# Optimization experiments

Measured on AMD Instinct MI355X. Metric: run time of the kernel, lower is better.

## Reference

```python
import jax, jax.numpy as jnp
import numpy as np

L, D, F, H, K, V, E = 15, 512, 2048, 64, 128, 30, 1024
DH = D // H  # 8
B, N = 8, 128


def _ln(x, s, b, eps=1e-5):
    m = x.mean(-1, keepdims=True)
    v = ((x - m) ** 2).mean(-1, keepdims=True)
    return (x - m) * jax.lax.rsqrt(v + eps) * s + b


def _gauss(x, mean, std):
    # matches torch.jit gaussian(): pi = 3.14159
    a = (2.0 * 3.14159) ** 0.5
    return jnp.exp(-0.5 * ((x - mean) / std) ** 2) / (a * std)


def setup_inputs() -> dict:
    key = jax.random.key(0)
    ks = iter(jax.random.split(key, 48))
    nrm = lambda shape, sc=0.02: jax.random.normal(next(ks), shape, jnp.float32) * sc
    zeros = lambda shape: jnp.zeros(shape, jnp.float32)
    ones = lambda shape: jnp.ones(shape, jnp.float32)
    return dict(
        src_tokens=jax.random.randint(next(ks), (B, N), 0, V),
        src_distance=jax.random.uniform(next(ks), (B, N, N), jnp.float32) * 3.0,
        src_edge_type=jax.random.randint(next(ks), (B, N, N), 0, E),
        token_embed=nrm((V, D)),
        gbf_means=jax.random.uniform(next(ks), (K,), jnp.float32, 0.0, 3.0),
        gbf_stds=jax.random.uniform(next(ks), (K,), jnp.float32, 0.0, 3.0),
        gbf_mul=ones((E, 1)),
        gbf_bias=zeros((E, 1)),
        proj_w1=nrm((K, K)), proj_b1=zeros((K,)),
        proj_w2=nrm((K, H)), proj_b2=zeros((H,)),
        emb_ln_s=ones((D,)), emb_ln_b=zeros((D,)),
        Wq=nrm((L, D, D)), bq=zeros((L, D)),
        Wk=nrm((L, D, D)), bk=zeros((L, D)),
        Wv=nrm((L, D, D)), bv=zeros((L, D)),
        Wo=nrm((L, D, D)), bo=zeros((L, D)),
        ln1_s=ones((L, D)), ln1_b=zeros((L, D)),
        ln2_s=ones((L, D)), ln2_b=zeros((L, D)),
        Wf1=nrm((L, D, F)), bf1=zeros((L, F)),
        Wf2=nrm((L, F, D)), bf2=zeros((L, D)),
        fin_ln_s=ones((D,)), fin_ln_b=zeros((D,)),
    )


def reference(src_tokens, src_distance, src_edge_type, token_embed,
              gbf_means, gbf_stds, gbf_mul, gbf_bias,
              proj_w1, proj_b1, proj_w2, proj_b2,
              emb_ln_s, emb_ln_b,
              Wq, bq, Wk, bk, Wv, bv, Wo, bo,
              ln1_s, ln1_b, ln2_s, ln2_b,
              Wf1, bf1, Wf2, bf2, fin_ln_s, fin_ln_b):
    # --- GaussianLayer: per-pair edge-type affine + K-kernel RBF -> [B,N,N,K]
    mul = gbf_mul[src_edge_type]          # [B,N,N,1]
    add = gbf_bias[src_edge_type]         # [B,N,N,1]
    g = mul * src_distance[..., None] + add
    std = jnp.abs(gbf_stds) + 1e-5
    g = _gauss(g, gbf_means, std)         # broadcast [B,N,N,1] vs [K] -> [B,N,N,K]
    # --- gbf_proj (NonLinearHead K->K->H) -> attention bias [B,H,N,N]
    hproj = jax.nn.gelu(g @ proj_w1 + proj_b1, approximate=False)
    bias0 = jnp.transpose(hproj @ proj_w2 + proj_b2, (0, 3, 1, 2))

    x = _ln(token_embed[src_tokens], emb_ln_s, emb_ln_b)  # [B,N,D]
    scale = DH ** -0.5

    def layer(carry, p):
        x, bias = carry
        wq, bq_, wk, bk_, wv, bv_, wo, bo_, s1, b1, s2, b2, wf1, bf1_, wf2, bf2_ = p
        # pre-LN self-attention with additive pair bias
        r = x
        y = _ln(x, s1, b1)
        q = (y @ wq + bq_).reshape(B, N, H, DH) * scale
        k = (y @ wk + bk_).reshape(B, N, H, DH)
        v = (y @ wv + bv_).reshape(B, N, H, DH)
        scores = jnp.einsum('bihd,bjhd->bhij', q, k) + bias  # [B,H,N,N]
        probs = jax.nn.softmax(scores, axis=-1)
        o = jnp.einsum('bhij,bjhd->bihd', probs, v).reshape(B, N, D)
        x = r + (o @ wo + bo_)
        # pre-LN FFN
        r = x
        y = _ln(x, s2, b2)
        y = jax.nn.gelu(y @ wf1 + bf1_, approximate=False) @ wf2 + bf2_
        # UniMol: pre-softmax scores feed the next layer as its pair bias
        return (r + y, scores), None

    (x, _), _ = jax.lax.scan(
        layer, (x, bias0),
        (Wq, bq, Wk, bk, Wv, bv, Wo, bo, ln1_s, ln1_b, ln2_s, ln2_b, Wf1, bf1, Wf2, bf2))
    return _ln(x, fin_ln_s, fin_ln_b)  # [B,N,D]
```

## Files before the change

### kernel.cpp

```cpp
#include <hip/hip_runtime.h>
#include <hip/hip_bf16.h>

#define Bv 8
#define Nv 128
#define Dv 512
#define Hv 64
#define DHv 8
#define Fv 2048
#define Lv 15
#define Kv 128

typedef unsigned short u16;
typedef __attribute__((ext_vector_type(8))) short s16x8;
typedef __attribute__((ext_vector_type(4))) float f32x4;

__device__ __forceinline__ float b2f(u16 u) {
    union { unsigned int i; float f; } w;
    w.i = ((unsigned int)u) << 16;
    return w.f;
}

__device__ __forceinline__ u16 f2b(float f) {
    __hip_bfloat16 h = __float2bfloat16(f);
    u16 u;
    __builtin_memcpy(&u, &h, 2);
    return u;
}

__device__ __forceinline__ bool probe_bf16(const void* p) {
    return ((const u16*)p)[0] == 0x3F80u;
}

__device__ __forceinline__ float ldv(const u16* p, size_t i)   { return b2f(p[i]); }
__device__ __forceinline__ float ldv(const float* p, size_t i) { return p[i]; }

__device__ __forceinline__ u16 ld16(const u16* p, size_t i)   { return p[i]; }
__device__ __forceinline__ u16 ld16(const float* p, size_t i) { return f2b(p[i]); }

__device__ __forceinline__ float erf_fast(float x) {
    float ax = fabsf(x);
    float tt = 1.0f / fmaf(0.3275911f, ax, 1.0f);
    float y = tt * fmaf(tt, fmaf(tt, fmaf(tt, fmaf(tt, 1.061405429f, -1.453152027f),
                                          1.421413741f), -0.284496736f), 0.254829592f);
    float r = 1.0f - y * __expf(-ax * ax);
    return copysignf(r, x);
}

__device__ __forceinline__ float geluf(float v) {
    return 0.5f * v * (1.0f + erf_fast(v * 0.70710678118654752f));
}

template<typename T>
__device__ __forceinline__ void gbf2_body(
    const T* dist, const int* etype, const T* means, const T* stds,
    const T* mulW, const T* addW, const T* w1, const T* b1w,
    const T* w2, const T* b2w, float* biasOut,
    float* xs, float* smean, float* sinv, u16* GA, u16* Bst)
{
    const int t = threadIdx.x;
    const int iq = blockIdx.x;
    const int j0 = blockIdx.y << 6;
    const int b = blockIdx.z;

    if (t < 64) {
        size_t pidx = ((size_t)(b * Nv + iq)) * Nv + j0 + t;
        int e = etype[pidx];
        xs[t] = ldv(dist, pidx) * ldv(mulW, e) + ldv(addW, e);
    } else if (t >= 128) {
        int k = t - 128;
        float sv = fabsf(ldv(stds, k)) + 1e-5f;
        smean[k] = ldv(means, k);
        sinv[k] = 1.0f / sv;
    }
    __syncthreads();

    const int w = t >> 6, l = t & 63;
    const int lg = l >> 4, lr = l & 15;
    const int wm = (w >> 1) << 5;
    const int wn1 = (w & 1) << 6;
    const int mt0 = wm >> 4;

    const int b1col = t & 127, b1lg0 = (t >> 7) << 1;

    s16x8 rb0, rb1;
    {
        union { s16x8 v; u16 u[8]; } p0, p1;
        #pragma unroll
        for (int j = 0; j < 8; j++) {
            p0.u[j] = ld16(w1, (size_t)((b1lg0 + 0) * 8 + j) * Kv + b1col);
            p1.u[j] = ld16(w1, (size_t)((b1lg0 + 1) * 8 + j) * Kv + b1col);
        }
        rb0 = p0.v; rb1 = p1.v;
    }

    {
        const int row = t & 63;
        const int kc = t >> 6;
        const float x = xs[row];
        const int mt = row >> 4, r = row & 15;
        #pragma unroll
        for (int lg2 = 0; lg2 < 4; lg2++) {
            union { s16x8 v; u16 u[8]; } pk;
            #pragma unroll
            for (int j = 0; j < 8; j++) {
                int k = kc * 32 + lg2 * 8 + j;
                float z = (x - smean[k]) * sinv[k];
                pk.u[j] = f2b(__expf(-0.5f * z * z) * (0.39894261f * sinv[k]));
            }
            *reinterpret_cast<s16x8*>(&GA[(((mt * 4 + kc) * 4 + lg2) * 16 + r) << 3]) = pk.v;
        }
    }
    __syncthreads();

    f32x4 acc1[2][4];
    #pragma unroll
    for (int mi = 0; mi < 2; mi++)
        #pragma unroll
        for (int ni = 0; ni < 4; ni++) acc1[mi][ni] = (f32x4){0.f, 0.f, 0.f, 0.f};

    for (int kc = 0; kc < 4; kc++) {
        *reinterpret_cast<s16x8*>(
            &Bst[((((b1col >> 4) * 4 + b1lg0 + 0) * 16 + (b1col & 15)) << 3)]) = rb0;
        *reinterpret_cast<s16x8*>(
            &Bst[((((b1col >> 4) * 4 + b1lg0 + 1) * 16 + (b1col & 15)) << 3)]) = rb1;
        __syncthreads();

        if (kc < 3) {
            union { s16x8 v; u16 u[8]; } p0, p1;
            #pragma unroll
            for (int j = 0; j < 8; j++) {
                p0.u[j] = ld16(w1, (size_t)((kc + 1) * 32 + (b1lg0 + 0) * 8 + j) * Kv + b1col);
                p1.u[j] = ld16(w1, (size_t)((kc + 1) * 32 + (b1lg0 + 1) * 8 + j) * Kv + b1col);
            }
            rb0 = p0.v; rb1 = p1.v;
        }

        s16x8 a0 = *reinterpret_cast<const s16x8*>(&GA[((((mt0 + 0) * 4 + kc) * 4 + lg) * 16 + lr) << 3]);
        s16x8 a1 = *reinterpret_cast<const s16x8*>(&GA[((((mt0 + 1) * 4 + kc) * 4 + lg) * 16 + lr) << 3]);
        #pragma unroll
        for (int ni = 0; ni < 4; ni++) {
            int nt = (wn1 >> 4) + ni;
            s16x8 bf = *reinterpret_cast<const s16x8*>(&Bst[((nt * 4 + lg) * 16 + lr) << 3]);
            acc1[0][ni] = __builtin_amdgcn_mfma_f32_16x16x32_bf16(a0, bf, acc1[0][ni], 0, 0, 0);
            acc1[1][ni] = __builtin_amdgcn_mfma_f32_16x16x32_bf16(a1, bf, acc1[1][ni], 0, 0, 0);
        }
        __syncthreads();
    }

    const int b2col = t & 63, b2lg = t >> 6;
    s16x8 rc;
    {
        union { s16x8 v; u16 u[8]; } pb;
        #pragma unroll
        for (int j = 0; j < 8; j++)
            pb.u[j] = ld16(w2, (size_t)(b2lg * 8 + j) * Hv + b2col);
        rc = pb.v;
    }

    #pragma unroll
    for (int mi = 0; mi < 2; mi++) {
        #pragma unroll
        for (int ni = 0; ni < 4; ni++) {
            int col = wn1 + ni * 16 + lr;
            float bb = ldv(b1w, col);
            #pragma unroll
            for (int i = 0; i < 4; i++) {
                int row = wm + mi * 16 + lg * 4 + i;
                float v = geluf(acc1[mi][ni][i] + bb);
                GA[((((row >> 4) * 4 + (col >> 5)) * 4 + ((col >> 3) & 3)) * 16 + (row & 15)) * 8 + (col & 7)] = f2b(v);
            }
        }
    }
    __syncthreads();

    const int wn2 = (w & 1) << 5;

    f32x4 acc2[2][2];
    #pragma unroll
    for (int mi = 0; mi < 2; mi++)
        #pragma unroll
        for (int ni = 0; ni < 2; ni++) acc2[mi][ni] = (f32x4){0.f, 0.f, 0.f, 0.f};

    for (int kc = 0; kc < 4; kc++) {
        *reinterpret_cast<s16x8*>(
            &Bst[((((b2col >> 4) * 4 + b2lg) * 16 + (b2col & 15)) << 3)]) = rc;
        __syncthreads();

        if (kc < 3) {
            union { s16x8 v; u16 u[8]; } pb;
            #pragma unroll
            for (int j = 0; j < 8; j++)
                pb.u[j] = ld16(w2, (size_t)((kc + 1) * 32 + b2lg * 8 + j) * Hv + b2col);
            rc = pb.v;
        }

        s16x8 a0 = *reinterpret_cast<const s16x8*>(&GA[((((mt0 + 0) * 4 + kc) * 4 + lg) * 16 + lr) << 3]);
        s16x8 a1 = *reinterpret_cast<const s16x8*>(&GA[((((mt0 + 1) * 4 + kc) * 4 + lg) * 16 + lr) << 3]);
        #pragma unroll
        for (int ni = 0; ni < 2; ni++) {
            int nt = (wn2 >> 4) + ni;
            s16x8 bf = *reinterpret_cast<const s16x8*>(&Bst[((nt * 4 + lg) * 16 + lr) << 3]);
            acc2[0][ni] = __builtin_amdgcn_mfma_f32_16x16x32_bf16(a0, bf, acc2[0][ni], 0, 0, 0);
            acc2[1][ni] = __builtin_amdgcn_mfma_f32_16x16x32_bf16(a1, bf, acc2[1][ni], 0, 0, 0);
        }
        __syncthreads();
    }

    #pragma unroll
    for (int mi = 0; mi < 2; mi++) {
        #pragma unroll
        for (int ni = 0; ni < 2; ni++) {
            int h = wn2 + ni * 16 + lr;
            int jb = wm + mi * 16 + lg * 4;
            float badd = ldv(b2w, h);
            size_t oidx = (((size_t)(b * Hv + h)) * Nv + iq) * Nv + j0 + jb;
            *reinterpret_cast<float4*>(&biasOut[oidx]) =
                make_float4(acc2[mi][ni][0] + badd, acc2[mi][ni][1] + badd,
                            acc2[mi][ni][2] + badd, acc2[mi][ni][3] + badd);
        }
    }
}

__global__ __launch_bounds__(256) void gbf2_k(
    const void* dist, const int* etype, const void* means, const void* stds,
    const void* mulW, const void* addW, const void* w1, const void* b1,
    const void* w2, const void* b2, float* biasOut, const void* probe)
{
    __shared__ float xs[64];
    __shared__ float smean[Kv];
    __shared__ float sinv[Kv];
    __shared__ __align__(16) u16 GA[8192];
    __shared__ __align__(16) u16 Bst[4096];
    if (probe_bf16(probe))
        gbf2_body<u16>((const u16*)dist, etype, (const u16*)means, (const u16*)stds,
                       (const u16*)mulW, (const u16*)addW, (const u16*)w1, (const u16*)b1,
                       (const u16*)w2, (const u16*)b2, biasOut, xs, smean, sinv, GA, Bst);
    else
        gbf2_body<float>((const float*)dist, etype, (const float*)means, (const float*)stds,
                         (const float*)mulW, (const float*)addW, (const float*)w1, (const float*)b1,
                         (const float*)w2, (const float*)b2, biasOut, xs, smean, sinv, GA, Bst);
}

__device__ __forceinline__ void block_stats_512(float x0, float x1, float& mean, float& rstd)
{
    float sum = x0 + x1, sq = x0 * x0 + x1 * x1;
    #pragma unroll
    for (int off = 32; off; off >>= 1) {
        sum += __shfl_xor(sum, off);
        sq  += __shfl_xor(sq, off);
    }
    __shared__ float ssum[4], ssq[4];
    int t = threadIdx.x;
    if ((t & 63) == 0) { ssum[t >> 6] = sum; ssq[t >> 6] = sq; }
    __syncthreads();
    sum = ssum[0] + ssum[1] + ssum[2] + ssum[3];
    sq  = ssq[0] + ssq[1] + ssq[2] + ssq[3];
    mean = sum * (1.0f / 512.0f);
    float var = sq * (1.0f / 512.0f) - mean * mean;
    rstd = rsqrtf(var + 1e-5f);
}

template<typename T>
__device__ __forceinline__ void embed_body(
    const int* toks, const T* emb, const T* sc, const T* bi, float* xout)
{
    int row = blockIdx.x, t = threadIdx.x;
    int tok = toks[row];
    float x0 = ldv(emb, (size_t)tok * Dv + t);
    float x1 = ldv(emb, (size_t)tok * Dv + t + 256);
    float mean, rstd;
    block_stats_512(x0, x1, mean, rstd);
    xout[(size_t)row * Dv + t]       = (x0 - mean) * rstd * ldv(sc, t) + ldv(bi, t);
    xout[(size_t)row * Dv + t + 256] = (x1 - mean) * rstd * ldv(sc, t + 256) + ldv(bi, t + 256);
}

__global__ __launch_bounds__(256) void embed_ln_k(
    const int* toks, const void* emb, const void* sc, const void* bi,
    float* xout, const void* probe)
{
    if (probe_bf16(probe))
        embed_body<u16>(toks, (const u16*)emb, (const u16*)sc, (const u16*)bi, xout);
    else
        embed_body<float>(toks, (const float*)emb, (const float*)sc, (const float*)bi, xout);
}

template<typename T>
__device__ __forceinline__ void ln_body(
    const float* xin, const T* sc, const T* bi, size_t pofs, u16* yout)
{
    int row = blockIdx.x, t = threadIdx.x;
    const float* xp = xin + (size_t)row * Dv;
    float x0 = xp[t], x1 = xp[t + 256];
    float mean, rstd;
    block_stats_512(x0, x1, mean, rstd);
    yout[(size_t)row * Dv + t]       = f2b((x0 - mean) * rstd * ldv(sc, pofs + t) + ldv(bi, pofs + t));
    yout[(size_t)row * Dv + t + 256] = f2b((x1 - mean) * rstd * ldv(sc, pofs + t + 256) + ldv(bi, pofs + t + 256));
}

__global__ __launch_bounds__(256) void ln_k(
    const float* xin, const void* sc, const void* bi, unsigned long long pofs,
    u16* yout, const void* probe)
{
    if (probe_bf16(probe))
        ln_body<u16>(xin, (const u16*)sc, (const u16*)bi, (size_t)pofs, yout);
    else
        ln_body<float>(xin, (const float*)sc, (const float*)bi, (size_t)pofs, yout);
}

template<typename T, bool OUT_BF>
__device__ __forceinline__ void final_ln_body(
    const float* xin, const T* sc, const T* bi, void* yout)
{
    int row = blockIdx.x, t = threadIdx.x;
    const float* xp = xin + (size_t)row * Dv;
    float x0 = xp[t], x1 = xp[t + 256];
    float mean, rstd;
    block_stats_512(x0, x1, mean, rstd);
    float o0 = (x0 - mean) * rstd * ldv(sc, t) + ldv(bi, t);
    float o1 = (x1 - mean) * rstd * ldv(sc, t + 256) + ldv(bi, t + 256);
    if (OUT_BF) {
        __hip_bfloat16* yp = (__hip_bfloat16*)yout;
        yp[(size_t)row * Dv + t]       = __float2bfloat16(o0);
        yp[(size_t)row * Dv + t + 256] = __float2bfloat16(o1);
    } else {
        float* yp = (float*)yout;
        yp[(size_t)row * Dv + t]       = o0;
        yp[(size_t)row * Dv + t + 256] = o1;
    }
}

__global__ __launch_bounds__(256) void final_ln_k(
    const float* xin, const void* sc, const void* bi, void* yout, const void* probe)
{
    if (probe_bf16(probe))
        final_ln_body<u16, true>(xin, (const u16*)sc, (const u16*)bi, yout);
    else
        final_ln_body<float, false>(xin, (const float*)sc, (const float*)bi, yout);
}

template<typename T>
__device__ __forceinline__ void gemm_mfma_body(
    const u16* A, const T* W, const T* bias, const float* R,
    void* C, int Nc, int Kc, int act, int res, int kbegin, int kend,
    int raw, int cbf, u16* Al, u16* Bl)
{
    const int tid = threadIdx.x;
    const int l = tid & 63, w = tid >> 6;
    const int wm = (w >> 1) << 5, wn = (w & 1) << 5;
    const int bm = blockIdx.y * 64, bn = blockIdx.x * 64;
    const int lg = l >> 4, lr = l & 15;
    const int mt0 = wm >> 4, nt0 = wn >> 4;

    f32x4 acc00 = {}, acc01 = {}, acc10 = {}, acc11 = {};

    const int arow = tid >> 2, akq = tid & 3;
    const u16* aGp = A + (size_t)(bm + arow) * Kc + (akq << 3);
    const int aL0 = ((((arow >> 4) * 2 + 0) * 4 + akq) * 16 + (arow & 15)) << 3;
    const int aL1 = ((((arow >> 4) * 2 + 1) * 4 + akq) * 16 + (arow & 15)) << 3;

    const int bcol = tid & 63;
    const int be = tid >> 6;
    const int bc = be >> 1, blg0 = (be & 1) << 1;
    const int bnt = bcol >> 4, bcl = bcol & 15;
    const int bL0 = (((bnt * 2 + bc) * 4 + blg0) * 16 + bcl) << 3;
    const int bL1 = (((bnt * 2 + bc) * 4 + blg0 + 1) * 16 + bcl) << 3;

    s16x8 ra0, ra1, rb0, rb1;
    ra0 = *reinterpret_cast<const s16x8*>(aGp + kbegin);
    ra1 = *reinterpret_cast<const s16x8*>(aGp + kbegin + 32);
    {
        union { s16x8 v; u16 u[8]; } p0, p1;
        #pragma unroll
        for (int j = 0; j < 8; j++) {
            p0.u[j] = ld16(W, (size_t)(kbegin + bc * 32 + blg0 * 8 + j) * Nc + bn + bcol);
            p1.u[j] = ld16(W, (size_t)(kbegin + bc * 32 + blg0 * 8 + 8 + j) * Nc + bn + bcol);
        }
        rb0 = p0.v; rb1 = p1.v;
    }

    for (int kt = kbegin; kt < kend; kt += 64) {
        *reinterpret_cast<s16x8*>(&Al[aL0]) = ra0;
        *reinterpret_cast<s16x8*>(&Al[aL1]) = ra1;
        *reinterpret_cast<s16x8*>(&Bl[bL0]) = rb0;
        *reinterpret_cast<s16x8*>(&Bl[bL1]) = rb1;
        __syncthreads();

        const int kn = kt + 64;
        if (kn < kend) {
            ra0 = *reinterpret_cast<const s16x8*>(aGp + kn);
            ra1 = *reinterpret_cast<const s16x8*>(aGp + kn + 32);
            union { s16x8 v; u16 u[8]; } p0, p1;
            #pragma unroll
            for (int j = 0; j < 8; j++) {
                p0.u[j] = ld16(W, (size_t)(kn + bc * 32 + blg0 * 8 + j) * Nc + bn + bcol);
                p1.u[j] = ld16(W, (size_t)(kn + bc * 32 + blg0 * 8 + 8 + j) * Nc + bn + bcol);
            }
            rb0 = p0.v; rb1 = p1.v;
        }

        #pragma unroll
        for (int c = 0; c < 2; c++) {
            s16x8 af0 = *reinterpret_cast<const s16x8*>(&Al[((((mt0 + 0) * 2 + c) * 4 + lg) * 16 + lr) << 3]);
            s16x8 af1 = *reinterpret_cast<const s16x8*>(&Al[((((mt0 + 1) * 2 + c) * 4 + lg) * 16 + lr) << 3]);
            s16x8 bf0 = *reinterpret_cast<const s16x8*>(&Bl[((((nt0 + 0) * 2 + c) * 4 + lg) * 16 + lr) << 3]);
            s16x8 bf1 = *reinterpret_cast<const s16x8*>(&Bl[((((nt0 + 1) * 2 + c) * 4 + lg) * 16 + lr) << 3]);
            acc00 = __builtin_amdgcn_mfma_f32_16x16x32_bf16(af0, bf0, acc00, 0, 0, 0);
            acc01 = __builtin_amdgcn_mfma_f32_16x16x32_bf16(af0, bf1, acc01, 0, 0, 0);
            acc10 = __builtin_amdgcn_mfma_f32_16x16x32_bf16(af1, bf0, acc10, 0, 0, 0);
            acc11 = __builtin_amdgcn_mfma_f32_16x16x32_bf16(af1, bf1, acc11, 0, 0, 0);
        }
        __syncthreads();
    }

    #pragma unroll
    for (int mi = 0; mi < 2; mi++) {
        #pragma unroll
        for (int i = 0; i < 4; i++) {
            const int row = bm + wm + mi * 16 + lg * 4 + i;
            const float* Rrow = res ? (R + (size_t)row * Nc) : nullptr;
            #pragma unroll
            for (int ni = 0; ni < 2; ni++) {
                const int col = bn + wn + ni * 16 + lr;
                float cv = (ni == 0) ? (mi == 0 ? acc00[i] : acc10[i])
                                     : (mi == 0 ? acc01[i] : acc11[i]);
                if (raw) {
                    ((float*)C)[(size_t)row * Nc + col] = cv;
                } else {
                    cv += ldv(bias, col);
                    if (act) cv = geluf(cv);
                    if (res) cv += Rrow[col];
                    if (cbf) ((u16*)C)[(size_t)row * Nc + col] = f2b(cv);
                    else     ((float*)C)[(size_t)row * Nc + col] = cv;
                }
            }
        }
    }
}

__global__ __launch_bounds__(256) void gemm_k(
    const u16* A, const void* W, unsigned long long wofs,
    const void* bias, unsigned long long bofs, const float* R,
    void* C, int Nc, int Kc, int act, int res, int cbf, const void* probe)
{
    __shared__ __align__(16) u16 Al[4096];
    __shared__ __align__(16) u16 Bl[4096];
    const int nz = gridDim.z, z = blockIdx.z;
    const int kchunk = Kc / nz;
    const int kbegin = z * kchunk, kend = kbegin + kchunk;
    const int raw = (nz > 1) ? 1 : 0;
    void* Cz = (char*)C + (size_t)z * ((size_t)gridDim.y * 64) * Nc * sizeof(float);
    if (probe_bf16(probe))
        gemm_mfma_body<u16>(A, (const u16*)W + wofs, (const u16*)bias + bofs, R, Cz,
                            Nc, Kc, act, res, kbegin, kend, raw, cbf, Al, Bl);
    else
        gemm_mfma_body<float>(A, (const float*)W + wofs, (const float*)bias + bofs, R, Cz,
                              Nc, Kc, act, res, kbegin, kend, raw, cbf, Al, Bl);
}

__global__ __launch_bounds__(256) void qkv_k(
    const u16* A,
    const void* W0, const void* W1p, const void* W2p, unsigned long long wofs,
    const void* b0, const void* b1p, const void* b2p, unsigned long long bofs,
    float* C0, float* C1, float* C2, const void* probe)
{
    __shared__ __align__(16) u16 Al[4096];
    __shared__ __align__(16) u16 Bl[4096];
    const int z = blockIdx.z;
    const void* W  = (z == 0) ? W0 : (z == 1) ? W1p : W2p;
    const void* bb = (z == 0) ? b0 : (z == 1) ? b1p : b2p;
    float* C       = (z == 0) ? C0 : (z == 1) ? C1 : C2;
    if (probe_bf16(probe))
        gemm_mfma_body<u16>(A, (const u16*)W + wofs, (const u16*)bb + bofs, nullptr, C,
                            Dv, Dv, 0, 0, 0, Dv, 0, 0, Al, Bl);
    else
        gemm_mfma_body<float>(A, (const float*)W + wofs, (const float*)bb + bofs, nullptr, C,
                              Dv, Dv, 0, 0, 0, Dv, 0, 0, Al, Bl);
}

template<typename T>
__device__ __forceinline__ void combln_body(
    const float* parts, const T* pbias, float* X,
    const T* lnS, const T* lnB, size_t pofs, u16* Y)
{
    const int t = threadIdx.x;
    const int rowb = t >> 7;
    const int col = (t & 127) << 2;
    const int row = (blockIdx.x << 1) + rowb;
    const size_t idx = (size_t)row * Dv + col;

    float4 sv = *reinterpret_cast<const float4*>(&parts[idx]);
    #pragma unroll
    for (int p = 1; p < 4; p++) {
        const float4 q2 = *reinterpret_cast<const float4*>(&parts[(size_t)p * 524288 + idx]);
        sv.x += q2.x; sv.y += q2.y; sv.z += q2.z; sv.w += q2.w;
    }
    sv.x += ldv(pbias, col);     sv.y += ldv(pbias, col + 1);
    sv.z += ldv(pbias, col + 2); sv.w += ldv(pbias, col + 3);
    const float4 r = *reinterpret_cast<const float4*>(&X[idx]);
    sv.x += r.x; sv.y += r.y; sv.z += r.z; sv.w += r.w;
    *reinterpret_cast<float4*>(&X[idx]) = sv;

    float sum = sv.x + sv.y + sv.z + sv.w;
    float sq  = sv.x * sv.x + sv.y * sv.y + sv.z * sv.z + sv.w * sv.w;
    #pragma unroll
    for (int off = 32; off; off >>= 1) {
        sum += __shfl_xor(sum, off);
        sq  += __shfl_xor(sq, off);
    }
    __shared__ float ssum[4], ssq[4];
    const int wv = t >> 6;
    if ((t & 63) == 0) { ssum[wv] = sum; ssq[wv] = sq; }
    __syncthreads();
    sum = ssum[rowb * 2] + ssum[rowb * 2 + 1];
    sq  = ssq[rowb * 2] + ssq[rowb * 2 + 1];
    const float mean = sum * (1.0f / 512.0f);
    const float var = sq * (1.0f / 512.0f) - mean * mean;
    const float rstd = rsqrtf(var + 1e-5f);

    ushort4 yv;
    yv.x = f2b((sv.x - mean) * rstd * ldv(lnS, pofs + col)     + ldv(lnB, pofs + col));
    yv.y = f2b((sv.y - mean) * rstd * ldv(lnS, pofs + col + 1) + ldv(lnB, pofs + col + 1));
    yv.z = f2b((sv.z - mean) * rstd * ldv(lnS, pofs + col + 2) + ldv(lnB, pofs + col + 2));
    yv.w = f2b((sv.w - mean) * rstd * ldv(lnS, pofs + col + 3) + ldv(lnB, pofs + col + 3));
    *reinterpret_cast<ushort4*>(&Y[idx]) = yv;
}

__global__ __launch_bounds__(256) void combln_k(
    const float* parts, const void* pbias, unsigned long long bofs, float* X,
    const void* lnS, const void* lnB, unsigned long long pofs, u16* Y,
    const void* probe)
{
    if (probe_bf16(probe))
        combln_body<u16>(parts, (const u16*)pbias + bofs, X,
                         (const u16*)lnS, (const u16*)lnB, (size_t)pofs, Y);
    else
        combln_body<float>(parts, (const float*)pbias + bofs, X,
                           (const float*)lnS, (const float*)lnB, (size_t)pofs, Y);
}

__global__ __launch_bounds__(512) void attn_k(
    const float* __restrict__ q, const float* __restrict__ k, const float* __restrict__ v,
    float* bias, u16* __restrict__ o)
{
    __shared__ __align__(16) float ks[Nv][DHv];
    __shared__ __align__(16) float vs[Nv][DHv];

    const int t = threadIdx.x;
    const int h = blockIdx.x;
    const int b = blockIdx.y;
    const int i = (blockIdx.z << 6) + (t >> 3);
    const int e = t & 7;
    const float scale = 0.35355339059327373f;

    const float* kh = k + (size_t)(b * Nv) * Dv + h * DHv;
    const float* vh = v + (size_t)(b * Nv) * Dv + h * DHv;

    {
        const int j = t >> 2, c = (t & 3) << 1;
        const float2 k2 = *reinterpret_cast<const float2*>(kh + (size_t)j * Dv + c);
        const float2 v2 = *reinterpret_cast<const float2*>(vh + (size_t)j * Dv + c);
        *reinterpret_cast<float2*>(&ks[j][c]) = k2;
        *reinterpret_cast<float2*>(&vs[j][c]) = v2;
    }

    const float* qp = q + (size_t)(b * Nv + i) * Dv + h * DHv;
    const float4 q0 = *reinterpret_cast<const float4*>(qp);
    const float4 q1 = *reinterpret_cast<const float4*>(qp + 4);

    float* bp = bias + (((size_t)(b * Hv + h)) * Nv + i) * Nv;

    float s[16];
    #pragma unroll
    for (int w = 0; w < 16; w++) s[w] = bp[(w << 3) + e];

    __syncthreads();

    float mx = -1e30f;
    #pragma unroll
    for (int w = 0; w < 16; w++) {
        const int j = (w << 3) + e;
        const float4 k0 = *reinterpret_cast<const float4*>(&ks[j][0]);
        const float4 k1 = *reinterpret_cast<const float4*>(&ks[j][4]);
        float d = q0.x * k0.x + q0.y * k0.y + q0.z * k0.z + q0.w * k0.w +
                  q1.x * k1.x + q1.y * k1.y + q1.z * k1.z + q1.w * k1.w;
        float val = s[w] + scale * d;
        s[w] = val;
        bp[j] = val;
        mx = fmaxf(mx, val);
    }

    mx = fmaxf(mx, __shfl_xor(mx, 1));
    mx = fmaxf(mx, __shfl_xor(mx, 2));
    mx = fmaxf(mx, __shfl_xor(mx, 4));

    float sum = 0.0f;
    #pragma unroll
    for (int w = 0; w < 16; w++) {
        s[w] = __expf(s[w] - mx);
        sum += s[w];
    }
    sum += __shfl_xor(sum, 1);
    sum += __shfl_xor(sum, 2);
    sum += __shfl_xor(sum, 4);
    const float inv = 1.0f / sum;

    float a0 = 0, a1 = 0, a2 = 0, a3 = 0, a4 = 0, a5 = 0, a6 = 0, a7 = 0;
    #pragma unroll
    for (int w = 0; w < 16; w++) {
        const int j = (w << 3) + e;
        const float4 v0 = *reinterpret_cast<const float4*>(&vs[j][0]);
        const float4 v1 = *reinterpret_cast<const float4*>(&vs[j][4]);
        const float p = s[w];
        a0 += p * v0.x; a1 += p * v0.y; a2 += p * v0.z; a3 += p * v0.w;
        a4 += p * v1.x; a5 += p * v1.y; a6 += p * v1.z; a7 += p * v1.w;
    }
    a0 += __shfl_xor(a0, 1); a0 += __shfl_xor(a0, 2); a0 += __shfl_xor(a0, 4);
    a1 += __shfl_xor(a1, 1); a1 += __shfl_xor(a1, 2); a1 += __shfl_xor(a1, 4);
    a2 += __shfl_xor(a2, 1); a2 += __shfl_xor(a2, 2); a2 += __shfl_xor(a2, 4);
    a3 += __shfl_xor(a3, 1); a3 += __shfl_xor(a3, 2); a3 += __shfl_xor(a3, 4);
    a4 += __shfl_xor(a4, 1); a4 += __shfl_xor(a4, 2); a4 += __shfl_xor(a4, 4);
    a5 += __shfl_xor(a5, 1); a5 += __shfl_xor(a5, 2); a5 += __shfl_xor(a5, 4);
    a6 += __shfl_xor(a6, 1); a6 += __shfl_xor(a6, 2); a6 += __shfl_xor(a6, 4);
    a7 += __shfl_xor(a7, 1); a7 += __shfl_xor(a7, 2); a7 += __shfl_xor(a7, 4);

    if (e == 0) {
        u16* op = o + (size_t)(b * Nv + i) * Dv + h * DHv;
        ushort4 o0 = { f2b(a0 * inv), f2b(a1 * inv), f2b(a2 * inv), f2b(a3 * inv) };
        ushort4 o1 = { f2b(a4 * inv), f2b(a5 * inv), f2b(a6 * inv), f2b(a7 * inv) };
        *reinterpret_cast<ushort4*>(op)     = o0;
        *reinterpret_cast<ushort4*>(op + 4) = o1;
    }
}

extern "C" void kernel_launch(void* const* d_in, const int* in_sizes, int n_in,
                              void* d_out, int out_size, void* d_ws, size_t ws_size,
                              hipStream_t stream)
{
    const int*  src_tokens = (const int*)d_in[0];
    const void* src_dist   = d_in[1];
    const int*  src_edge   = (const int*)d_in[2];
    const void* token_emb  = d_in[3];
    const void* gbf_means  = d_in[4];
    const void* gbf_stds   = d_in[5];
    const void* gbf_mul    = d_in[6];
    const void* gbf_bias   = d_in[7];
    const void* pw1        = d_in[8];
    const void* pb1        = d_in[9];
    const void* pw2        = d_in[10];
    const void* pb2        = d_in[11];
    const void* embs       = d_in[12];
    const void* embb       = d_in[13];
    const void* Wq         = d_in[14];
    const void* bq         = d_in[15];
    const void* Wk         = d_in[16];
    const void* bk         = d_in[17];
    const void* Wv         = d_in[18];
    const void* bvp        = d_in[19];
    const void* Wo         = d_in[20];
    const void* bo         = d_in[21];
    const void* ln1s       = d_in[22];
    const void* ln1b       = d_in[23];
    const void* ln2s       = d_in[24];
    const void* ln2b       = d_in[25];
    const void* Wf1        = d_in[26];
    const void* bf1        = d_in[27];
    const void* Wf2        = d_in[28];
    const void* bf2        = d_in[29];
    const void* fins       = d_in[30];
    const void* finb       = d_in[31];
    const void* probe      = embs;

    float* ws   = (float*)d_ws;
    float* x    = ws;
    float* y    = x  + 524288;
    float* qb   = y  + 524288;
    float* kb   = qb + 524288;
    float* vb   = kb + 524288;
    float* ob   = vb + 524288;
    float* hb   = ob + 524288;
    u16*   hbf  = (u16*)hb;
    u16*   ybf  = (u16*)(hb + 1048576);
    u16*   obf  = (u16*)(hb + 1310720);
    float* bias = hb + 2097152;

    gbf2_k<<<dim3(Nv, 2, Bv), 256, 0, stream>>>(
        src_dist, src_edge, gbf_means, gbf_stds, gbf_mul, gbf_bias,
        pw1, pb1, pw2, pb2, bias, probe);
    embed_ln_k<<<Bv * Nv, 256, 0, stream>>>(src_tokens, token_emb, embs, embb, x, probe);
    ln_k<<<Bv * Nv, 256, 0, stream>>>(x, ln1s, ln1b, 0ull, ybf, probe);

    dim3 gQKV(512 / 64, 1024 / 64, 3);
    dim3 gS4(512 / 64, 1024 / 64, 4);
    dim3 gF1(2048 / 64, 1024 / 64);
    for (int l = 0; l < Lv; l++) {
        unsigned long long wofs  = (unsigned long long)l * Dv * Dv;
        unsigned long long wofsF = (unsigned long long)l * Dv * Fv;
        unsigned long long dof   = (unsigned long long)l * Dv;
        unsigned long long fof   = (unsigned long long)l * Fv;
        unsigned long long nofs  = (l + 1 < Lv) ? (unsigned long long)(l + 1) * Dv : 0ull;

        qkv_k<<<gQKV, 256, 0, stream>>>(ybf, Wq, Wk, Wv, wofs, bq, bk, bvp, dof,
                                        qb, kb, vb, probe);
        attn_k<<<dim3(Hv, Bv, 2), 512, 0, stream>>>(qb, kb, vb, bias, obf);
        gemm_k<<<gS4, 256, 0, stream>>>(obf, Wo, wofs, bo, dof, nullptr, y, 512, 512, 0, 0, 0, probe);
        combln_k<<<512, 256, 0, stream>>>(y, bo, dof, x, ln2s, ln2b, dof, ybf, probe);
        gemm_k<<<gF1, 256, 0, stream>>>(ybf, Wf1, wofsF, bf1, fof, nullptr, hbf, 2048, 512, 1, 0, 1, probe);
        gemm_k<<<gS4, 256, 0, stream>>>(hbf, Wf2, wofsF, bf2, fof, nullptr, y, 512, 2048, 0, 0, 0, probe);
        combln_k<<<512, 256, 0, stream>>>(y, bf2, dof, x, ln1s, ln1b, nofs, ybf, probe);
    }
    final_ln_k<<<Bv * Nv, 256, 0, stream>>>(x, fins, finb, d_out, probe);
}
```

Baseline: 1.460 ms.

## Double-buffer GEMM LDS tiles and split-K the QKV projection into attention

The shared GEMM body now ping-pongs between two LDS buffers, so the next K-tile is written to the alternate buffer after the MFMAs and only one barrier is needed per iteration. The QKV kernel is split along K into two halves (six z-slices instead of three), which doubles the number of blocks. It writes raw partial sums into spare workspace buffers. The attention kernel then adds the two partials and the q/k/v biases when it loads them. This trades extra LDS per block (lower occupancy) and extra partial-sum traffic for more parallelism and less barrier stalling.

```diff
diff --git a/kernel.cpp b/kernel.cpp
--- a/kernel.cpp
+++ b/kernel.cpp
@@ -377,16 +377,17 @@
         }
         rb0 = p0.v; rb1 = p1.v;
     }
-
+    *reinterpret_cast<s16x8*>(&Al[aL0]) = ra0;
+    *reinterpret_cast<s16x8*>(&Al[aL1]) = ra1;
+    *reinterpret_cast<s16x8*>(&Bl[bL0]) = rb0;
+    *reinterpret_cast<s16x8*>(&Bl[bL1]) = rb1;
+    __syncthreads();
+
+    int cur = 0;
     for (int kt = kbegin; kt < kend; kt += 64) {
-        *reinterpret_cast<s16x8*>(&Al[aL0]) = ra0;
-        *reinterpret_cast<s16x8*>(&Al[aL1]) = ra1;
-        *reinterpret_cast<s16x8*>(&Bl[bL0]) = rb0;
-        *reinterpret_cast<s16x8*>(&Bl[bL1]) = rb1;
-        __syncthreads();
-
         const int kn = kt + 64;
-        if (kn < kend) {
+        const bool more = kn < kend;
+        if (more) {
             ra0 = *reinterpret_cast<const s16x8*>(aGp + kn);
             ra1 = *reinterpret_cast<const s16x8*>(aGp + kn + 32);
             union { s16x8 v; u16 u[8]; } p0, p1;
@@ -398,18 +399,28 @@
             rb0 = p0.v; rb1 = p1.v;
         }
 
+        const int co = cur << 12;
         #pragma unroll
         for (int c = 0; c < 2; c++) {
-            s16x8 af0 = *reinterpret_cast<const s16x8*>(&Al[((((mt0 + 0) * 2 + c) * 4 + lg) * 16 + lr) << 3]);
-            s16x8 af1 = *reinterpret_cast<const s16x8*>(&Al[((((mt0 + 1) * 2 + c) * 4 + lg) * 16 + lr) << 3]);
-            s16x8 bf0 = *reinterpret_cast<const s16x8*>(&Bl[((((nt0 + 0) * 2 + c) * 4 + lg) * 16 + lr) << 3]);
-            s16x8 bf1 = *reinterpret_cast<const s16x8*>(&Bl[((((nt0 + 1) * 2 + c) * 4 + lg) * 16 + lr) << 3]);
+            s16x8 af0 = *reinterpret_cast<const s16x8*>(&Al[co + (((((mt0 + 0) * 2 + c) * 4 + lg) * 16 + lr) << 3)]);
+            s16x8 af1 = *reinterpret_cast<const s16x8*>(&Al[co + (((((mt0 + 1) * 2 + c) * 4 + lg) * 16 + lr) << 3)]);
+            s16x8 bf0 = *reinterpret_cast<const s16x8*>(&Bl[co + (((((nt0 + 0) * 2 + c) * 4 + lg) * 16 + lr) << 3)]);
+            s16x8 bf1 = *reinterpret_cast<const s16x8*>(&Bl[co + (((((nt0 + 1) * 2 + c) * 4 + lg) * 16 + lr) << 3)]);
             acc00 = __builtin_amdgcn_mfma_f32_16x16x32_bf16(af0, bf0, acc00, 0, 0, 0);
             acc01 = __builtin_amdgcn_mfma_f32_16x16x32_bf16(af0, bf1, acc01, 0, 0, 0);
             acc10 = __builtin_amdgcn_mfma_f32_16x16x32_bf16(af1, bf0, acc10, 0, 0, 0);
             acc11 = __builtin_amdgcn_mfma_f32_16x16x32_bf16(af1, bf1, acc11, 0, 0, 0);
         }
-        __syncthreads();
+
+        if (more) {
+            const int no = (cur ^ 1) << 12;
+            *reinterpret_cast<s16x8*>(&Al[no + aL0]) = ra0;
+            *reinterpret_cast<s16x8*>(&Al[no + aL1]) = ra1;
+            *reinterpret_cast<s16x8*>(&Bl[no + bL0]) = rb0;
+            *reinterpret_cast<s16x8*>(&Bl[no + bL1]) = rb1;
+            __syncthreads();
+            cur ^= 1;
+        }
     }
 
     #pragma unroll
@@ -442,8 +453,8 @@
     const void* bias, unsigned long long bofs, const float* R,
     void* C, int Nc, int Kc, int act, int res, int cbf, const void* probe)
 {
-    __shared__ __align__(16) u16 Al[4096];
-    __shared__ __align__(16) u16 Bl[4096];
+    __shared__ __align__(16) u16 Al[8192];
+    __shared__ __align__(16) u16 Bl[8192];
     const int nz = gridDim.z, z = blockIdx.z;
     const int kchunk = Kc / nz;
     const int kbegin = z * kchunk, kend = kbegin + kchunk;
@@ -460,21 +471,24 @@
 __global__ __launch_bounds__(256) void qkv_k(
     const u16* A,
     const void* W0, const void* W1p, const void* W2p, unsigned long long wofs,
-    const void* b0, const void* b1p, const void* b2p, unsigned long long bofs,
-    float* C0, float* C1, float* C2, const void* probe)
-{
-    __shared__ __align__(16) u16 Al[4096];
-    __shared__ __align__(16) u16 Bl[4096];
+    float* q0, float* q1, float* k0, float* k1, float* v0, float* v1,
+    const void* probe)
+{
+    __shared__ __align__(16) u16 Al[8192];
+    __shared__ __align__(16) u16 Bl[8192];
     const int z = blockIdx.z;
-    const void* W  = (z == 0) ? W0 : (z == 1) ? W1p : W2p;
-    const void* bb = (z == 0) ? b0 : (z == 1) ? b1p : b2p;
-    float* C       = (z == 0) ? C0 : (z == 1) ? C1 : C2;
+    const int g = z >> 1, half = z & 1;
+    const void* W  = (g == 0) ? W0 : (g == 1) ? W1p : W2p;
+    float* C       = (g == 0) ? (half ? q1 : q0)
+                   : (g == 1) ? (half ? k1 : k0)
+                              : (half ? v1 : v0);
+    const int kbegin = half * 256, kend = kbegin + 256;
     if (probe_bf16(probe))
-        gemm_mfma_body<u16>(A, (const u16*)W + wofs, (const u16*)bb + bofs, nullptr, C,
-                            Dv, Dv, 0, 0, 0, Dv, 0, 0, Al, Bl);
+        gemm_mfma_body<u16>(A, (const u16*)W + wofs, (const u16*)nullptr, nullptr, C,
+                            Dv, Dv, 0, 0, kbegin, kend, 1, 0, Al, Bl);
     else
-        gemm_mfma_body<float>(A, (const float*)W + wofs, (const float*)bb + bofs, nullptr, C,
-                              Dv, Dv, 0, 0, 0, Dv, 0, 0, Al, Bl);
+        gemm_mfma_body<float>(A, (const float*)W + wofs, (const float*)nullptr, nullptr, C,
+                              Dv, Dv, 0, 0, kbegin, kend, 1, 0, Al, Bl);
 }
 
 template<typename T>
@@ -539,12 +553,16 @@
 }
 
 __global__ __launch_bounds__(512) void attn_k(
-    const float* __restrict__ q, const float* __restrict__ k, const float* __restrict__ v,
-    float* bias, u16* __restrict__ o)
+    const float* __restrict__ q0p, const float* __restrict__ q1p,
+    const float* __restrict__ k0p, const float* __restrict__ k1p,
+    const float* __restrict__ v0p, const float* __restrict__ v1p,
+    const void* bqv, const void* bkv, const void* bvv, unsigned long long bofs,
+    float* bias, u16* __restrict__ o, const void* probe)
 {
     __shared__ __align__(16) float ks[Nv][DHv];
     __shared__ __align__(16) float vs[Nv][DHv];
 
+    const bool bf = probe_bf16(probe);
     const int t = threadIdx.x;
     const int h = blockIdx.x;
     const int b = blockIdx.y;
@@ -552,20 +570,38 @@
     const int e = t & 7;
     const float scale = 0.35355339059327373f;
 
-    const float* kh = k + (size_t)(b * Nv) * Dv + h * DHv;
-    const float* vh = v + (size_t)(b * Nv) * Dv + h * DHv;
-
     {
         const int j = t >> 2, c = (t & 3) << 1;
-        const float2 k2 = *reinterpret_cast<const float2*>(kh + (size_t)j * Dv + c);
-        const float2 v2 = *reinterpret_cast<const float2*>(vh + (size_t)j * Dv + c);
-        *reinterpret_cast<float2*>(&ks[j][c]) = k2;
-        *reinterpret_cast<float2*>(&vs[j][c]) = v2;
-    }
-
-    const float* qp = q + (size_t)(b * Nv + i) * Dv + h * DHv;
-    const float4 q0 = *reinterpret_cast<const float4*>(qp);
-    const float4 q1 = *reinterpret_cast<const float4*>(qp + 4);
+        const size_t off = (size_t)(b * Nv + j) * Dv + h * DHv + c;
+        const float2 ka = *reinterpret_cast<const float2*>(k0p + off);
+        const float2 kb2 = *reinterpret_cast<const float2*>(k1p + off);
+        const float2 va = *reinterpret_cast<const float2*>(v0p + off);
+        const float2 vb2 = *reinterpret_cast<const float2*>(v1p + off);
+        const size_t bci = (size_t)bofs + h * DHv + c;
+        const float bk0 = bf ? b2f(((const u16*)bkv)[bci])     : ((const float*)bkv)[bci];
+        const float bk1 = bf ? b2f(((const u16*)bkv)[bci + 1]) : ((const float*)bkv)[bci + 1];
+        const float bv0 = bf ? b2f(((const u16*)bvv)[bci])     : ((const float*)bvv)[bci];
+        const float bv1 = bf ? b2f(((const u16*)bvv)[bci + 1]) : ((const float*)bvv)[bci + 1];
+        ks[j][c]     = ka.x + kb2.x + bk0;
+        ks[j][c + 1] = ka.y + kb2.y + bk1;
+        vs[j][c]     = va.x + vb2.x + bv0;
+        vs[j][c + 1] = va.y + vb2.y + bv1;
+    }
+
+    const size_t qoff = (size_t)(b * Nv + i) * Dv + h * DHv;
+    const float4 qa0 = *reinterpret_cast<const float4*>(q0p + qoff);
+    const float4 qa1 = *reinterpret_cast<const float4*>(q0p + qoff + 4);
+    const float4 qc0 = *reinterpret_cast<const float4*>(q1p + qoff);
+    const float4 qc1 = *reinterpret_cast<const float4*>(q1p + qoff + 4);
+    float bq[8];
+    #pragma unroll
+    for (int d = 0; d < 8; d++)
+        bq[d] = bf ? b2f(((const u16*)bqv)[(size_t)bofs + h * DHv + d])
+                   : ((const float*)bqv)[(size_t)bofs + h * DHv + d];
+    const float4 q0 = make_float4(qa0.x + qc0.x + bq[0], qa0.y + qc0.y + bq[1],
+                                  qa0.z + qc0.z + bq[2], qa0.w + qc0.w + bq[3]);
+    const float4 q1 = make_float4(qa1.x + qc1.x + bq[4], qa1.y + qc1.y + bq[5],
+                                  qa1.z + qc1.z + bq[6], qa1.w + qc1.w + bq[7]);
 
     float* bp = bias + (((size_t)(b * Hv + h)) * Nv + i) * Nv;
 
@@ -681,6 +717,7 @@
     u16*   hbf  = (u16*)hb;
     u16*   ybf  = (u16*)(hb + 1048576);
     u16*   obf  = (u16*)(hb + 1310720);
+    float* hbt  = hb + 1572864;
     float* bias = hb + 2097152;
 
     gbf2_k<<<dim3(Nv, 2, Bv), 256, 0, stream>>>(
@@ -689,7 +726,7 @@
     embed_ln_k<<<Bv * Nv, 256, 0, stream>>>(src_tokens, token_emb, embs, embb, x, probe);
     ln_k<<<Bv * Nv, 256, 0, stream>>>(x, ln1s, ln1b, 0ull, ybf, probe);
 
-    dim3 gQKV(512 / 64, 1024 / 64, 3);
+    dim3 gQKV(512 / 64, 1024 / 64, 6);
     dim3 gS4(512 / 64, 1024 / 64, 4);
     dim3 gF1(2048 / 64, 1024 / 64);
     for (int l = 0; l < Lv; l++) {
@@ -699,9 +736,10 @@
         unsigned long long fof   = (unsigned long long)l * Fv;
         unsigned long long nofs  = (l + 1 < Lv) ? (unsigned long long)(l + 1) * Dv : 0ull;
 
-        qkv_k<<<gQKV, 256, 0, stream>>>(ybf, Wq, Wk, Wv, wofs, bq, bk, bvp, dof,
-                                        qb, kb, vb, probe);
-        attn_k<<<dim3(Hv, Bv, 2), 512, 0, stream>>>(qb, kb, vb, bias, obf);
+        qkv_k<<<gQKV, 256, 0, stream>>>(ybf, Wq, Wk, Wv, wofs,
+                                        qb, y, kb, ob, vb, hbt, probe);
+        attn_k<<<dim3(Hv, Bv, 2), 512, 0, stream>>>(
+            qb, y, kb, ob, vb, hbt, bq, bk, bvp, dof, bias, obf, probe);
         gemm_k<<<gS4, 256, 0, stream>>>(obf, Wo, wofs, bo, dof, nullptr, y, 512, 512, 0, 0, 0, probe);
         combln_k<<<512, 256, 0, stream>>>(y, bo, dof, x, ln2s, ln2b, dof, ybf, probe);
         gemm_k<<<gF1, 256, 0, stream>>>(ybf, Wf1, wofsF, bf1, fof, nullptr, hbf, 2048, 512, 1, 0, 1, probe);
```

Result: no change. 1.481 ms (+1.5%).
